# Performance work log

Measured on AMD Instinct MI355X. Metric: run time of the kernel, lower is better.

The kernel has to match this reference:

```python
import jax, jax.numpy as jnp
import numpy as np

B, N, C_IN, C_EMB, G = 16, 1024, 16, 64, 128
NEG = -1e12


def _lap(m):
    # m @ D^-1/2, transpose, @ D^-1/2  (matches torch code incl. transpose)
    d = jnp.sum(m, axis=1) ** -0.5
    return (m * d[None, :]).T * d[None, :]


def setup_inputs():
    key = jax.random.key(0)
    ks = jax.random.split(key, 16)
    f = jax.random.normal
    return {
        'x': f(ks[0], (B, C_IN, N), jnp.float32),
        'ct': f(ks[1], (B, C_EMB, N), jnp.float32),
        'graph_data': jax.random.uniform(ks[2], (2, N, N), dtype=jnp.float32),
        'emb_w': f(ks[3], (C_EMB, C_IN)) / np.sqrt(C_IN).astype(np.float32),
        'emb_b': f(ks[4], (C_EMB,)) * 0.01,
        'emb2_w': f(ks[5], (N, N)) / np.sqrt(N).astype(np.float32),
        'emb2_b': f(ks[6], (N,)) * 0.01,
        'att_W': f(ks[7], (C_EMB, C_EMB)) / np.sqrt(C_EMB).astype(np.float32),
        'att_a': f(ks[8], (2 * C_EMB, 1)) / np.sqrt(2 * C_EMB).astype(np.float32),
        'att_GL': f(ks[9], (N, G)) / np.sqrt(G).astype(np.float32),
        'uai_w': f(ks[10], (C_EMB, C_EMB)) / np.sqrt(C_EMB).astype(np.float32),
        'uai_b': f(ks[11], (C_EMB,)) * 0.01,
        'lin1_w': f(ks[12], (C_EMB, C_EMB)) / np.sqrt(C_EMB).astype(np.float32),
        'lin2_w': f(ks[13], (C_EMB, C_EMB)) / np.sqrt(C_EMB).astype(np.float32),
        'lin2_b': f(ks[14], (C_EMB,)) * 0.01,
        'ln_w': jnp.ones((C_EMB, N), jnp.float32),
        'ln_b': jnp.zeros((C_EMB, N), jnp.float32),
    }


def reference(x, ct, graph_data, emb_w, emb_b, emb2_w, emb2_b, att_W, att_a,
              att_GL, uai_w, uai_b, lin1_w, lin2_w, lin2_b, ln_w, ln_b):
    # emb: Conv1d k=1 -> leaky_relu -> Linear over node axis N
    h0 = jax.nn.leaky_relu(jnp.einsum('bcn,ec->ben', x, emb_w) + emb_b[None, :, None])
    h0 = jnp.einsum('ben,mn->bem', h0, emb2_w) + emb2_b[None, None, :]
    inp = jnp.swapaxes(h0, 1, 2)  # [B,N,C']

    # InterpositionAttention (repeat/cat factorized: e_ij = leakyrelu(a1.h_i + a2.h_j))
    eye = jnp.eye(N, dtype=x.dtype)
    adj_att = jax.nn.softmax(jax.nn.relu(att_GL @ att_GL.T), axis=-1) + eye
    h = inp @ att_W  # [B,N,C']
    e = jax.nn.leaky_relu((h @ att_a[:C_EMB]) + jnp.swapaxes(h @ att_a[C_EMB:], 1, 2))  # [B,N,N]
    att = jax.nn.softmax(jnp.where(adj_att > 0, e, NEG), axis=2)
    x_att = jnp.swapaxes(jax.nn.relu(att @ h), 1, 2)  # [B,C',N]

    # UAI module (eval mode: dropout off -> all MC samples equal -> sigma = 0)
    mu = jnp.swapaxes(x_att, 1, 2) @ uai_w.T + uai_b  # [B,N,C']
    x_uai = jnp.swapaxes(mu, 1, 2)  # [B,C',N]

    g1 = _lap(graph_data[0] + eye)
    g2 = _lap(graph_data[1] + eye)

    # learned adjacency from pairwise squared distances (cdist p=2, squared)
    xf = jnp.swapaxes(x_uai, 1, 2)  # [B,N,C']
    sq = jnp.sum(xf * xf, axis=-1)
    d2 = jnp.maximum(sq[:, :, None] + sq[:, None, :] - 2.0 * (xf @ jnp.swapaxes(xf, 1, 2)), 0.0)
    gl = jax.nn.softmax(jnp.exp(-d2 / (2.0 * C_EMB)) + eye, axis=-1)  # sigma^2 = emb_size

    def ln(z):  # LayerNorm over last two dims [C', N]
        m = jnp.mean(z, axis=(1, 2), keepdims=True)
        v = jnp.var(z, axis=(1, 2), keepdims=True)
        return (z - m) / jnp.sqrt(v + 1e-5) * ln_w + ln_b

    l1 = lambda z: jnp.einsum('oc,bcn->bon', lin1_w, z)
    l2 = lambda z: jnp.einsum('oc,bcn->bon', lin2_w, z) + lin2_b[None, :, None]

    x_new = ln(l1(x_uai) @ gl + l1(l1(x_uai) @ g1) @ g2)
    ft = jax.nn.gelu(ln(l2(x_uai) @ gl + l2(l2(x_uai) @ g1) @ g2), approximate=False)
    rt = ft  # rt is computed by the identical expression (dropout off)

    ct_new = ft * ct + x_new - ft * x_new
    ht = rt * jax.nn.elu(ct_new) + x_uai - rt * x_uai
    return (ht, ct_new)
```

## Files before the change

### kernel.cpp

```cpp
#include <hip/hip_runtime.h>
#include <math.h>

typedef unsigned short u16;
typedef __attribute__((ext_vector_type(8))) short short8;
typedef __attribute__((ext_vector_type(4))) float floatx4;

constexpr int BATCH = 16;
constexpr int NI = 1024;
constexpr int CE = 64;
constexpr int CI = 16;
constexpr long long NN2  = (long long)NI * NI;
constexpr long long BCN  = (long long)BATCH * CE * NI;
constexpr long long BNv  = (long long)BATCH * NI;
constexpr long long BNN  = (long long)BATCH * NI * NI;
constexpr long long S1 = (long long)CE * NI;
constexpr long long S2 = 2 * S1;
constexpr int ZERON = (int)(2 * BNv + 80);

__device__ __forceinline__ float lrelu01(float x) { return x > 0.f ? x : 0.01f * x; }

__device__ __forceinline__ u16 f2bf(float f) {
  unsigned u = __builtin_bit_cast(unsigned, f);
  return (u16)((u + 0x7fffu + ((u >> 16) & 1u)) >> 16);
}
__device__ __forceinline__ float bf2f(u16 h) {
  unsigned u = ((unsigned)h) << 16;
  return __builtin_bit_cast(float, u);
}
__device__ __forceinline__ unsigned fkey(float f) {
  unsigned u = __builtin_bit_cast(unsigned, f);
  return (u & 0x80000000u) ? ~u : (u | 0x80000000u);
}
__device__ __forceinline__ float funkey(unsigned k) {
  unsigned u = (k & 0x80000000u) ? (k & 0x7fffffffu) : ~k;
  return __builtin_bit_cast(float, u);
}

__device__ __forceinline__ void gload16(const u16* g, u16* l) {
  __builtin_amdgcn_global_load_lds(
      (const __attribute__((address_space(1))) void*)g,
      (__attribute__((address_space(3))) void*)l, 16, 0, 0);
}

__device__ __forceinline__ void pipe_fence() {
  asm volatile("s_waitcnt vmcnt(0) lgkmcnt(0)" ::: "memory");
  __builtin_amdgcn_sched_barrier(0);
  __builtin_amdgcn_s_barrier();
  __builtin_amdgcn_sched_barrier(0);
}

template<int N>
__device__ __forceinline__ void fence_bar() {
  __builtin_amdgcn_sched_barrier(0);
  if constexpr (N == 0) asm volatile("s_waitcnt vmcnt(0)" ::: "memory");
  else if constexpr (N == 1) asm volatile("s_waitcnt vmcnt(1)" ::: "memory");
  else if constexpr (N == 2) asm volatile("s_waitcnt vmcnt(2)" ::: "memory");
  else if constexpr (N == 3) asm volatile("s_waitcnt vmcnt(3)" ::: "memory");
  else if constexpr (N == 4) asm volatile("s_waitcnt vmcnt(4)" ::: "memory");
  else if constexpr (N == 6) asm volatile("s_waitcnt vmcnt(6)" ::: "memory");
  else if constexpr (N == 8) asm volatile("s_waitcnt vmcnt(8)" ::: "memory");
  else asm volatile("s_waitcnt vmcnt(0)" ::: "memory");
  __builtin_amdgcn_s_barrier();
  __builtin_amdgcn_sched_barrier(0);
}

template<int BM, int BN, int MODE>
__global__ __launch_bounds__(256) void mgemm(
    const u16* __restrict__ Ag, const u16* __restrict__ B1g, const u16* __restrict__ B2g,
    int K1, int K, int lda, int ldb, long long bsA, long long bsB1,
    float* __restrict__ Cf, u16* __restrict__ Cb, int ldc, long long bsC,
    const float* __restrict__ aux1, const float* __restrict__ aux2,
    const float* __restrict__ aux3, const float* __restrict__ aux4,
    float* __restrict__ Zout)
{
  constexpr int RM = BM / 2, RN = BN / 2, MI = RM / 16, NJ = RN / 16;
  constexpr bool PIPE3 = (MODE == 5 || MODE == 14 || MODE == 15);
  constexpr int DEPTH = (MODE == 5) ? 4 : 3;
  constexpr int NBUF = PIPE3 ? DEPTH : (MODE == 13 ? 2 : 1);
  constexpr int NLA = (BM * 8) / 256;
  constexpr int NLB = (BN * 8) / 256;
  constexpr int L = (MODE == 13) ? NLB : (NLA + NLB);
  __shared__ __align__(16) u16 As[NBUF * BM * 64];
  __shared__ __align__(16) u16 Bs[NBUF * BN * 64];
  __shared__ __align__(16) u16 xa[MODE == 13 ? 32 * 72 : 1];
  const int tid = threadIdx.x;
  int z, n0, r0;
  if constexpr (MODE == 15) {
    const int id = blockIdx.x;
    if (id >= 512) {
      const int m = id - 512;
      float s = 0.f, sv = 0.f;
      for (int n = tid; n < NI; n += 256) {
        float g = aux3[(long long)m * NI + n] * aux2[n];
        s += g;
        sv = fmaf(g, aux1[n], sv);
      }
      float* r1 = (float*)As;
      float* r2 = (float*)As + 256;
      r1[tid] = s; r2[tid] = sv; __syncthreads();
      for (int st = 128; st > 0; st >>= 1) {
        if (tid < st) { r1[tid] += r1[tid + st]; r2[tid] += r2[tid + st]; }
        __syncthreads();
      }
      if (tid == 0) {
        float dm = aux2[m];
        Cf[m] = dm * (r1[0] + dm);
        Zout[m] = dm * (r2[0] + dm * aux1[m]);
      }
      return;
    }
    z = 0; n0 = (id & 15) * BN; r0 = (id >> 4) * BM;
  } else {
    z = blockIdx.z; n0 = blockIdx.x * BN; r0 = blockIdx.y * BM;
  }
  const u16* Ab = Ag + (long long)z * bsA + (long long)r0 * lda;
  const u16* Bb1 = B1g + (long long)z * bsB1 + (long long)n0 * ldb;
  const int lane = tid & 63;
  const int wid = tid >> 6;
  const int wr = wid >> 1, wc = wid & 1;
  const int q = lane >> 4, mlow = lane & 15;
  const int wbase = tid & ~63;

  floatx4 acc[MI][NJ] = {};
  float zp0 = 0.f;

  float s1r_13 = 0.f, mr_13 = 0.f;
  const float* s2z_13 = nullptr;
  float4 sa, sb;
  if constexpr (MODE == 13) {
    const float* s1z = aux2 + (long long)z * NI;
    s2z_13 = aux3 + (long long)z * NI;
    const float mb = funkey(((const unsigned*)aux4)[z]);
    s1r_13 = s1z[r0 + (tid >> 3)];
    mr_13 = lrelu01(s1r_13 + mb);
  }

  auto stageAB = [&](int buf, int k0) {
    if constexpr (MODE != 13) {
      const u16* Asrc = Ab + k0;
#pragma unroll
      for (int s = 0; s < NLA; s++) {
        int cid = tid + s * 256;
        int r = cid >> 3, cc = cid & 7;
        gload16(Asrc + (long long)r * lda + ((cc ^ (r & 7)) << 3),
                As + buf * (BM * 64) + ((wbase + s * 256) << 3));
      }
    }
    const u16* Bsrc = (k0 < K1) ? (Bb1 + k0)
                                : (B2g + (long long)n0 * ldb + (k0 - K1));
#pragma unroll
    for (int s = 0; s < NLB; s++) {
      int cid = tid + s * 256;
      int r = cid >> 3, cc = cid & 7;
      gload16(Bsrc + (long long)r * ldb + ((cc ^ (r & 7)) << 3),
              Bs + buf * (BN * 64) + ((wbase + s * 256) << 3));
    }
  };

  auto agen_ld = [&](int k0) {
    const float* sp = s2z_13 + k0 + (tid & 7) * 8;
    sa = *(const float4*)sp;
    sb = *(const float4*)(sp + 4);
  };
  auto agen_st = [&](int buf) {
    int r = tid >> 3, craw = tid & 7;
    float p0 = __expf(lrelu01(s1r_13 + sa.x) - mr_13);
    float p1 = __expf(lrelu01(s1r_13 + sa.y) - mr_13);
    float p2 = __expf(lrelu01(s1r_13 + sa.z) - mr_13);
    float p3 = __expf(lrelu01(s1r_13 + sa.w) - mr_13);
    float p4 = __expf(lrelu01(s1r_13 + sb.x) - mr_13);
    float p5 = __expf(lrelu01(s1r_13 + sb.y) - mr_13);
    float p6 = __expf(lrelu01(s1r_13 + sb.z) - mr_13);
    float p7 = __expf(lrelu01(s1r_13 + sb.w) - mr_13);
    zp0 += p0 + p1 + p2 + p3 + p4 + p5 + p6 + p7;
    uint4 v;
    v.x = (unsigned)f2bf(p0) | ((unsigned)f2bf(p1) << 16);
    v.y = (unsigned)f2bf(p2) | ((unsigned)f2bf(p3) << 16);
    v.z = (unsigned)f2bf(p4) | ((unsigned)f2bf(p5) << 16);
    v.w = (unsigned)f2bf(p6) | ((unsigned)f2bf(p7) << 16);
    *(uint4*)&As[buf * (BM * 64) + (r * 8 + (craw ^ (r & 7))) * 8] = v;
  };

  auto compute_tile = [&](int buf) {
#pragma unroll
    for (int kh = 0; kh < 2; kh++) {
      const int kc = kh * 4 + q;
      short8 afr[MI], bfr[NJ];
#pragma unroll
      for (int i = 0; i < MI; i++) {
        int row = wr * RM + i * 16 + mlow;
        afr[i] = *(const short8*)&As[buf * (BM * 64) + (row * 8 + (kc ^ (row & 7))) * 8];
      }
#pragma unroll
      for (int j = 0; j < NJ; j++) {
        int row = wc * RN + j * 16 + mlow;
        bfr[j] = *(const short8*)&Bs[buf * (BN * 64) + (row * 8 + (kc ^ (row & 7))) * 8];
      }
#pragma unroll
      for (int i = 0; i < MI; i++)
#pragma unroll
        for (int j = 0; j < NJ; j++)
          acc[i][j] = __builtin_amdgcn_mfma_f32_16x16x32_bf16(afr[i], bfr[j], acc[i][j], 0, 0, 0);
    }
  };

  if constexpr (PIPE3) {
    const int nk = K >> 6;
#pragma unroll
    for (int p = 0; p < DEPTH - 1; p++) stageAB(p, p << 6);
    fence_bar<(DEPTH - 2) * L>();
    int cur = 0, stg = DEPTH - 1;
    for (int ki = 0; ki < nk; ki++) {
      if (ki + DEPTH - 1 < nk) stageAB(stg, (ki + DEPTH - 1) << 6);
      compute_tile(cur);
      if (ki + 1 < nk) {
        const int rem = nk - 1 - ki;
        const int u = (rem < DEPTH - 1) ? rem : (DEPTH - 1);
        if constexpr (DEPTH == 4) {
          if (u == 3) fence_bar<2 * L>();
          else if (u == 2) fence_bar<L>();
          else fence_bar<0>();
        } else {
          if (u == 2) fence_bar<L>();
          else fence_bar<0>();
        }
      }
      cur++; if (cur == NBUF) cur = 0;
      stg++; if (stg == NBUF) stg = 0;
    }
    __syncthreads();
  } else if constexpr (MODE == 13) {
    agen_ld(0);
    stageAB(0, 0);
    agen_st(0);
    pipe_fence();
    int cur = 0;
    for (int k0 = 0; k0 < K; k0 += 64) {
      if (k0 + 64 < K) {
        agen_ld(k0 + 64);
        stageAB(cur ^ 1, k0 + 64);
        agen_st(cur ^ 1);
      }
      compute_tile(cur);
      pipe_fence();
      cur ^= 1;
    }
  } else {
    for (int k0 = 0; k0 < K; k0 += 64) {
      stageAB(0, k0);
      __syncthreads();
      compute_tile(0);
      __syncthreads();
    }
  }

  if constexpr (MODE == 3) {
    const float* sqb = aux1 + (long long)z * NI;
#pragma unroll
    for (int i = 0; i < MI; i++) {
#pragma unroll
      for (int rg = 0; rg < 4; rg++) {
        int r = r0 + wr * RM + i * 16 + q * 4 + rg;
        float sqi = sqb[r];
        float rsum = 0.f;
#pragma unroll
        for (int j = 0; j < NJ; j++) {
          int ncol = n0 + wc * RN + j * 16 + mlow;
          float d2 = fmaxf(sqi + sqb[ncol] - 2.f * acc[i][j][rg], 0.f);
          float w = __expf(__expf(-d2 * (1.f / 128.f)) + (r == ncol ? 1.f : 0.f) - 2.f);
          Cb[(long long)z * bsC + (long long)r * ldc + ncol] = f2bf(w);
          rsum += w;
        }
        rsum += __shfl_xor(rsum, 1);
        rsum += __shfl_xor(rsum, 2);
        rsum += __shfl_xor(rsum, 4);
        rsum += __shfl_xor(rsum, 8);
        if (mlow == 0) atomicAdd(&Zout[(long long)z * NI + r], rsum);
      }
    }
  } else if constexpr (MODE == 14) {
    float ps1 = 0.f, ps2 = 0.f;
#pragma unroll
    for (int i = 0; i < MI; i++) {
#pragma unroll
      for (int rg = 0; rg < 4; rg++) {
        int r = wr * RM + i * 16 + q * 4 + rg;
        int ncol = n0 + wc * RN + mlow;
        float v = acc[i][0][rg] + aux3[r] * aux1[ncol];
        Cb[(long long)z * bsC + (long long)r * ldc + ncol] = f2bf(v);
        ps1 = fmaf(v, aux2[r], ps1);
        ps2 = fmaf(v, aux2[64 + r], ps2);
      }
    }
    ps1 += __shfl_xor(ps1, 16); ps1 += __shfl_xor(ps1, 32);
    ps2 += __shfl_xor(ps2, 16); ps2 += __shfl_xor(ps2, 32);
    float* sred = (float*)As;
    const int col = wc * RN + mlow;
    if (q == 0) { sred[col * 2 + wr] = ps1; sred[64 + col * 2 + wr] = ps2; }
    __syncthreads();
    if (tid < 32) {
      float v1 = sred[tid * 2] + sred[tid * 2 + 1];
      float v2 = sred[64 + tid * 2] + sred[64 + tid * 2 + 1];
      Cf[(long long)z * NI + n0 + tid] = v1;
      Zout[(long long)z * NI + n0 + tid] = v2;
      float mx = v2;
      for (int off = 1; off < 32; off <<= 1) mx = fmaxf(mx, __shfl_xor(mx, off));
      if (tid == 0) atomicMax((unsigned*)B2g + z, fkey(mx));
    }
  } else if constexpr (MODE == 13) {
    float* zred = (float*)xa;
    float* zinv = (float*)xa + 256;
    zred[(tid >> 3) * 8 + (tid & 7)] = zp0;
    __syncthreads();
    if (tid < 32) {
      float sum = 0.f;
#pragma unroll
      for (int j = 0; j < 8; j++) sum += zred[tid * 8 + j];
      zinv[tid] = 1.f / sum;
    }
    __syncthreads();
    float zr[4];
#pragma unroll
    for (int rg = 0; rg < 4; rg++) zr[rg] = zinv[wr * 16 + q * 4 + rg];
    __syncthreads();
#pragma unroll
    for (int j = 0; j < NJ; j++) {
#pragma unroll
      for (int rg = 0; rg < 4; rg++) {
        int row = wr * 16 + q * 4 + rg;
        int col = wc * RN + j * 16 + mlow;
        float v = fmaxf(acc[0][j][rg] * zr[rg], 0.f);
        xa[row * 72 + col] = f2bf(v);
      }
    }
#pragma unroll
    for (int s = 0; s < 2; s++) {
      int cid = tid + s * 256;
      int r = cid >> 3, cc = cid & 7;
      gload16(B2g + r * 64 + ((cc ^ (r & 7)) << 3),
              Bs + ((wbase + s * 256) << 3));
    }
    __syncthreads();
    floatx4 acc2[2] = {};
#pragma unroll
    for (int kh = 0; kh < 2; kh++) {
      const int kc = kh * 4 + q;
      short8 a2 = *(const short8*)&xa[(wr * 16 + mlow) * 72 + kc * 8];
#pragma unroll
      for (int j = 0; j < 2; j++) {
        int orow = wc * 32 + j * 16 + mlow;
        short8 b2 = *(const short8*)&Bs[(orow * 8 + (kc ^ (orow & 7))) * 8];
        acc2[j] = __builtin_amdgcn_mfma_f32_16x16x32_bf16(a2, b2, acc2[j], 0, 0, 0);
      }
    }
#pragma unroll
    for (int rg = 0; rg < 4; rg++) {
      int row = r0 + wr * 16 + q * 4 + rg;
      float sqp = 0.f;
#pragma unroll
      for (int j = 0; j < 2; j++) {
        int o = wc * 32 + j * 16 + mlow;
        float v = acc2[j][rg] + aux1[o];
        Cb[(long long)z * bsC + (long long)row * ldc + o] = f2bf(v);
        sqp = fmaf(v, v, sqp);
      }
      sqp += __shfl_xor(sqp, 1);
      sqp += __shfl_xor(sqp, 2);
      sqp += __shfl_xor(sqp, 4);
      sqp += __shfl_xor(sqp, 8);
      if (mlow == 0) atomicAdd(&Zout[(long long)z * NI + row], sqp);
    }
  } else if constexpr (MODE == 5) {
    float ts = 0.f, tss = 0.f;
#pragma unroll
    for (int i = 0; i < MI; i++) {
#pragma unroll
      for (int j = 0; j < NJ; j++) {
#pragma unroll
        for (int rg = 0; rg < 4; rg++) {
          int r = r0 + wr * RM + i * 16 + q * 4 + rg;
          int ncol = n0 + wc * RN + j * 16 + mlow;
          float v = acc[i][j][rg];
          v += aux3[r] * aux1[ncol] + aux4[r] * aux2[ncol];
          Cb[(long long)z * bsC + (long long)r * ldc + ncol] = f2bf(v);
          ts += v;
          tss = fmaf(v, v, tss);
        }
      }
    }
    float* red = (float*)As;
    red[tid] = ts; red[256 + tid] = tss;
    __syncthreads();
    for (int st = 128; st > 0; st >>= 1) {
      if (tid < st) { red[tid] += red[tid + st]; red[256 + tid] += red[256 + tid + st]; }
      __syncthreads();
    }
    if (tid == 0) {
      const int half = r0 >> 6;
      atomicAdd(&Zout[z * 2 + half], red[0]);
      atomicAdd(&Zout[32 + z * 2 + half], red[256]);
    }
  } else {
#pragma unroll
    for (int i = 0; i < MI; i++) {
#pragma unroll
      for (int j = 0; j < NJ; j++) {
#pragma unroll
        for (int rg = 0; rg < 4; rg++) {
          int r = r0 + wr * RM + i * 16 + q * 4 + rg;
          int ncol = n0 + wc * RN + j * 16 + mlow;
          float v = acc[i][j][rg];
          if constexpr (MODE == 4) {
            int blk = r >> 6, oo = r & 63;
            int drow = ((blk & 1) << 6) + oo;
            if (blk < 2) v = (v + aux3[drow]) / aux1[(long long)z * NI + ncol];
            Cb[(long long)z * bsC + (long long)drow * 2048 + (long long)(blk >> 1) * 1024 + ncol] =
                f2bf(v);
          } else {
            Cb[(long long)z * bsC + (long long)r * ldc + ncol] = f2bf(v);
          }
        }
      }
    }
  }
}

__global__ __launch_bounds__(256) void lap_rowsum(const float* __restrict__ gd,
                                                  float* __restrict__ dr,
                                                  float* __restrict__ zero)
{
  if (blockIdx.x >= 2048) {
    int i = (blockIdx.x - 2048) * 256 + threadIdx.x;
    if (i < ZERON) zero[i] = 0.f;
    return;
  }
  const int ki = blockIdx.x;
  const float* row = gd + (long long)ki * NI;
  float s = 0.f;
  for (int j = threadIdx.x; j < NI; j += 256) s += row[j];
  __shared__ float red[256];
  red[threadIdx.x] = s; __syncthreads();
  for (int st = 128; st > 0; st >>= 1) {
    if (threadIdx.x < st) red[threadIdx.x] += red[threadIdx.x + st];
    __syncthreads();
  }
  if (threadIdx.x == 0) dr[ki] = rsqrtf(red[0] + 1.f);
}

__global__ __launch_bounds__(256) void mega_prep(
    const float* __restrict__ l1w, const float* __restrict__ l2w,
    const float* __restrict__ l2b, const float* __restrict__ uaiw,
    const float* __restrict__ attW,
    u16* __restrict__ stack4, float* __restrict__ rb2ext, float* __restrict__ rl2ext,
    u16* __restrict__ uaiw_bf, u16* __restrict__ attwT_bf, float* __restrict__ wcs,
    const float* __restrict__ emb2w, u16* __restrict__ emb2w_bf,
    const float* __restrict__ x, const float* __restrict__ ew,
    const float* __restrict__ eb, u16* __restrict__ h0aT,
    const float* __restrict__ gd, const float* __restrict__ dsum,
    u16* __restrict__ g2t, u16* __restrict__ g1,
    float* __restrict__ cs1)
{
  __shared__ float sm[1092];
  const int bid = blockIdx.x;
  const int t = threadIdx.x;
  if (bid < 98) {
    const int gid = bid * 256 + t;
    if (gid < 4096) {
      stack4[gid] = f2bf(l1w[gid]);
    } else if (gid < 8192) {
      stack4[gid] = f2bf(l2w[gid - 4096]);
    } else if (gid < 12288) {
      int tt = gid - 8192, o = tt >> 6, m = tt & 63;
      float s = 0.f;
      for (int c = 0; c < 64; c++) s = fmaf(l1w[o * 64 + c], l1w[c * 64 + m], s);
      stack4[gid] = f2bf(s);
    } else if (gid < 16384) {
      int tt = gid - 12288, o = tt >> 6, m = tt & 63;
      float s = 0.f;
      for (int c = 0; c < 64; c++) s = fmaf(l2w[o * 64 + c], l2w[c * 64 + m], s);
      stack4[gid] = f2bf(s);
    } else if (gid < 16512) {
      int r = gid - 16384;
      rb2ext[r] = (r < 64) ? 0.f : l2b[r - 64];
    } else if (gid < 16640) {
      int r = gid - 16512;
      float v = 0.f;
      if (r >= 64) { int o = r - 64; for (int c = 0; c < 64; c++) v = fmaf(l2w[o * 64 + c], l2b[c], v); }
      rl2ext[r] = v;
    } else if (gid < 20736) {
      uaiw_bf[gid - 16640] = f2bf(uaiw[gid - 16640]);
    } else if (gid < 24832) {
      int idx = gid - 20736;
      int c = idx >> 6, e = idx & 63;
      attwT_bf[idx] = f2bf(attW[e * 64 + c]);
    } else if (gid < 24896) {
      int c = gid - 24832;
      float s = 0.f;
      for (int e = 0; e < 64; e++) s += attW[e * 64 + c];
      wcs[c] = s;
    }
  } else if (bid < 4194) {
    const long long i = (long long)(bid - 98) * 256 + t;
    emb2w_bf[i] = f2bf(emb2w[i]);
  } else if (bid < 4450) {
    const int sub = bid - 4194;
    const int b = sub >> 4;
    const int nc = (sub & 15) * 64;
    float* we = sm;
    float* be = sm + 1024;
    for (int i = t; i < 1024; i += 256) we[i] = ew[i];
    if (t < 64) be[t] = eb[t];
    __syncthreads();
    const int n = nc + (t >> 2);
    const int e0 = (t & 3) * 16;
    const float* xb = x + (long long)b * CI * NI + n;
    float xv[16];
#pragma unroll
    for (int c = 0; c < CI; c++) xv[c] = xb[(long long)c * NI];
    u16 out16[16];
#pragma unroll
    for (int ee = 0; ee < 16; ee++) {
      const int e = e0 + ee;
      float a = be[e];
#pragma unroll
      for (int c = 0; c < CI; c++) a = fmaf(xv[c], we[e * 16 + c], a);
      out16[ee] = f2bf(lrelu01(a));
    }
    u16* dst = h0aT + (long long)b * S1 + (long long)n * 64 + e0;
    *(uint4*)dst = *(uint4*)out16;
    *(uint4*)(dst + 8) = *(uint4*)(out16 + 8);
  } else if (bid < 8546) {
    const long long idx = (long long)(bid - 4450) * 256 + t;
    const int m = (int)(idx >> 10), j = (int)(idx & 1023);
    const float* d = dsum + NI;
    float v = (gd[NN2 + idx] + (m == j ? 1.f : 0.f)) * d[m] * d[j];
    g2t[idx] = f2bf(v);
  } else if (bid < 9570) {
    const int sub = bid - 8546;
    const int bx = (sub & 31) * 32, by = (sub >> 5) * 32;
    const int lx = t & 31, ly = t >> 5;
    float* tile = sm;
    for (int yy = ly; yy < 32; yy += 8)
      tile[yy * 33 + lx] = gd[(long long)(by + yy) * NI + bx + lx];
    __syncthreads();
    for (int yy = ly; yy < 32; yy += 8) {
      const int i = bx + yy, j = by + lx;
      float v = (tile[lx * 33 + yy] + (i == j ? 1.f : 0.f)) * dsum[i] * dsum[j];
      g1[(long long)i * NI + j] = f2bf(v);
    }
  } else {
    const int n = bid - 9570;
    float s = 0.f;
    for (int i = t; i < NI; i += 256) s = fmaf(gd[(long long)n * NI + i], dsum[i], s);
    float* red = sm;
    red[t] = s; __syncthreads();
    for (int st = 128; st > 0; st >>= 1) {
      if (t < st) red[t] += red[t + st];
      __syncthreads();
    }
    if (t == 0) cs1[n] = dsum[n] * (red[0] + dsum[n]);
  }
}

__global__ __launch_bounds__(512) void ln_final_t(const u16* __restrict__ T,
                                                  const float* __restrict__ stats,
                                                  const float* __restrict__ lnw,
                                                  const float* __restrict__ lnb,
                                                  const float* __restrict__ ct,
                                                  const u16* __restrict__ xuT,
                                                  float* __restrict__ outp)
{
  __shared__ float xs[64 * 65];
  const int blk = blockIdx.x;
  const int b = blk >> 4;
  const int n0 = (blk & 15) << 6;
  const int t = threadIdx.x;
  const int tc = t & 63, tr = t >> 6;
#pragma unroll
  for (int i = 0; i < 8; i++) {
    int nn = i * 8 + tr;
    xs[tc * 65 + nn] = bf2f(xuT[((long long)b << 16) + (long long)(n0 + nn) * 64 + tc]);
  }
  __syncthreads();
  const float inv_n = 1.f / 65536.f;
  const float m0 = stats[b * 2] * inv_n;
  const float m1 = stats[b * 2 + 1] * inv_n;
  const float rs0 = rsqrtf(fmaxf(stats[32 + b * 2] * inv_n - m0 * m0, 0.f) + 1e-5f);
  const float rs1 = rsqrtf(fmaxf(stats[32 + b * 2 + 1] * inv_n - m1 * m1, 0.f) + 1e-5f);
#pragma unroll
  for (int j = 0; j < 8; j++) {
    const int c = j * 8 + tr;
    const int n = n0 + tc;
    const int rem = c * NI + n;
    const long long toff = (long long)b * S2 + rem;
    const float t0 = bf2f(T[toff]);
    const float t1 = bf2f(T[toff + S1]);
    const float w = lnw[rem], bb = lnb[rem];
    const float xn = (t0 - m0) * rs0 * w + bb;
    float ft = (t1 - m1) * rs1 * w + bb;
    ft = 0.5f * ft * (1.f + erff(ft * 0.70710678118654752f));
    const float u = xs[c * 65 + tc];
    const long long oidx = ((long long)b << 16) + rem;
    const float cn = fmaf(ft, ct[oidx] - xn, xn);
    const float el = cn > 0.f ? cn : expm1f(cn);
    outp[oidx] = fmaf(ft, el - u, u);
    outp[BCN + oidx] = cn;
  }
}

extern "C" void kernel_launch(void* const* d_in, const int* in_sizes, int n_in,
                              void* d_out, int out_size, void* d_ws, size_t ws_size,
                              hipStream_t stream)
{
  (void)in_sizes; (void)n_in; (void)out_size; (void)ws_size;
  const float* x      = (const float*)d_in[0];
  const float* ct     = (const float*)d_in[1];
  const float* gdata  = (const float*)d_in[2];
  const float* emb_w  = (const float*)d_in[3];
  const float* emb_b  = (const float*)d_in[4];
  const float* emb2_w = (const float*)d_in[5];
  const float* emb2_b = (const float*)d_in[6];
  const float* att_W  = (const float*)d_in[7];
  const float* att_a  = (const float*)d_in[8];
  const float* uai_w  = (const float*)d_in[10];
  const float* uai_b  = (const float*)d_in[11];
  const float* lin1_w = (const float*)d_in[12];
  const float* lin2_w = (const float*)d_in[13];
  const float* lin2_b = (const float*)d_in[14];
  const float* ln_w   = (const float*)d_in[15];
  const float* ln_b   = (const float*)d_in[16];
  float* outp = (float*)d_out;

  float* ws = (float*)d_ws;
  long long o = 0;
  auto af = [&](long long n) { float* p = ws + o; o += (n + 63) & ~63LL; return p; };
  auto au = [&](long long n) { return (u16*)af((n + 1) / 2); };

  float* s1      = af(BNv);
  float* s2      = af(BNv);
  float* dsum    = af(2 * NI);
  float* cs1v    = af(NI);
  float* cs2v    = af(NI);
  float* v2v     = af(NI);
  float* rb2ext  = af(128);
  float* rl2ext  = af(128);
  float* wcs     = af(64);
  float* zeroreg = af(ZERON);
  float* Zgl     = zeroreg;
  float* sqv     = zeroreg + BNv;
  float* stats   = zeroreg + 2 * BNv;
  unsigned* s2mU = (unsigned*)(stats + 64);
  u16* Tacc      = au(S2 * BATCH);
  u16* emb2w_bf  = au(NN2);
  u16* h0aTb     = au(S1 * BATCH);
  u16* ybf       = au(S1 * BATCH);
  u16* hTb       = au(S1 * BATCH);
  u16* xuaiTb    = au(S1 * BATCH);
  u16* g1b       = au(NN2);
  u16* g2tb      = au(NN2);
  u16* G12b      = au(NN2);
  u16* Abig      = au((long long)BATCH * 128 * 2048);
  u16* stack4    = au(256 * 64);
  u16* uaiw_bf   = au(CE * CE);
  u16* attwT_bf  = au(CE * CE);
  u16* bigW      = au(BNN);

  lap_rowsum<<<2048 + (ZERON + 255) / 256, 256, 0, stream>>>(gdata, dsum, zeroreg);

  mega_prep<<<10594, 256, 0, stream>>>(
      lin1_w, lin2_w, lin2_b, uai_w, att_W,
      stack4, rb2ext, rl2ext, uaiw_bf, attwT_bf, wcs,
      emb2_w, emb2w_bf, x, emb_w, emb_b, h0aTb,
      gdata, dsum, g2tb, g1b, cs1v);

  mgemm<32, 64, 15><<<1536, 256, 0, stream>>>(
      g2tb, g1b, nullptr, NI, NI, NI, NI, 0, 0,
      cs2v, G12b, NI, 0, cs1v, dsum + NI, gdata + NN2, nullptr, v2v);

  mgemm<64, 32, 6><<<dim3(32, 1, BATCH), 256, 0, stream>>>(
      attwT_bf, h0aTb, nullptr, CE, CE, CE, CE, 0, S1,
      nullptr, ybf, NI, S1, nullptr, nullptr, nullptr, nullptr, nullptr);

  mgemm<64, 32, 14><<<dim3(32, 1, BATCH), 256, 0, stream>>>(
      ybf, emb2w_bf, (const u16*)s2mU, NI, NI, NI, NI, S1, 0,
      s1, hTb, NI, S1, emb2_b, att_a, wcs, nullptr, s2);

  mgemm<32, 64, 13><<<dim3(1, 32, BATCH), 256, 0, stream>>>(
      hTb, hTb, uaiw_bf, NI, NI, NI, NI, 0, S1,
      nullptr, xuaiTb, CE, S1, uai_b, s1, s2, (const float*)s2mU, sqv);

  mgemm<128, 128, 3><<<dim3(8, 8, BATCH), 256, 0, stream>>>(
      xuaiTb, xuaiTb, nullptr, CE, CE, CE, CE, S1, S1,
      nullptr, bigW, NI, NN2, sqv, nullptr, nullptr, nullptr, Zgl);

  mgemm<64, 64, 4><<<dim3(16, 4, BATCH), 256, 0, stream>>>(
      stack4, xuaiTb, nullptr, CE, CE, CE, CE, 0, S1,
      nullptr, Abig, 0, (long long)128 * 2048, Zgl, nullptr, rb2ext, nullptr, nullptr);

  mgemm<64, 64, 5><<<dim3(16, 2, BATCH), 256, 0, stream>>>(
      Abig, bigW, G12b, NI, 2 * NI, 2048, NI, (long long)128 * 2048, NN2,
      nullptr, Tacc, NI, S2, cs2v, v2v, rb2ext, rl2ext, stats);

  ln_final_t<<<256, 512, 0, stream>>>(Tacc, stats, ln_w, ln_b, ct, xuaiTb, outp);
}
```

Baseline: 229.6 us.

## Merge attention-weight GEMM into G12 launch, retile distance GEMM, XCD-swizzle final GEMM

Folds the small MODE 6 attention-weight projection GEMM into the MODE 15 launch as an extra set of 512 blocks. This removes one kernel launch and lets that work overlap with the G12 product and the column-sum blocks. The pairwise-distance GEMM (MODE 3) drops from 128x128 to 64x64 tiles, giving four times as many blocks. The final fused GEMM (MODE 5) now runs on a 1D grid whose block IDs are remapped so that blocks sharing a batch land on the same XCD, improving L2 locality. The risks are the pointer-offset trick that reaches ybf relative to G12b, and the smaller tiles cutting per-block reuse.

```diff
diff --git a/kernel.cpp b/kernel.cpp
--- a/kernel.cpp
+++ b/kernel.cpp
@@ -84,10 +84,11 @@
   __shared__ __align__(16) u16 Bs[NBUF * BN * 64];
   __shared__ __align__(16) u16 xa[MODE == 13 ? 32 * 72 : 1];
   const int tid = threadIdx.x;
-  int z, n0, r0;
+  int z, n0, r0, job15 = 0;
+  long long cboff = 0;
   if constexpr (MODE == 15) {
     const int id = blockIdx.x;
-    if (id >= 512) {
+    if (id >= 512 && id < 1536) {
       const int m = id - 512;
       float s = 0.f, sv = 0.f;
       for (int n = tid; n < NI; n += 256) {
@@ -109,12 +110,37 @@
       }
       return;
     }
-    z = 0; n0 = (id & 15) * BN; r0 = (id >> 4) * BM;
+    if (id >= 1536) {
+      const int id2 = id - 1536;
+      job15 = 2;
+      z = id2 >> 5; r0 = (id2 & 1) * BM; n0 = ((id2 >> 1) & 15) * BN;
+    } else {
+      z = 0; n0 = (id & 15) * BN; r0 = (id >> 4) * BM;
+    }
+  } else if constexpr (MODE == 5) {
+    const int fid = blockIdx.x;
+    const int xcd = fid & 7, idx = fid >> 3;
+    const int code = (idx >> 4) * 8 + xcd;
+    z = code >> 1; r0 = (code & 1) * BM; n0 = (idx & 15) * BN;
   } else {
     z = blockIdx.z; n0 = blockIdx.x * BN; r0 = blockIdx.y * BM;
   }
-  const u16* Ab = Ag + (long long)z * bsA + (long long)r0 * lda;
-  const u16* Bb1 = B1g + (long long)z * bsB1 + (long long)n0 * ldb;
+  int Kv = K, K1v = K1, ldav = lda, ldbv = ldb;
+  const u16 *Ab, *Bb1;
+  if constexpr (MODE == 15) {
+    if (job15 == 2) {
+      Kv = 64; K1v = 128; ldav = 64; ldbv = 64;
+      Ab = B2g + (long long)r0 * 64;
+      Bb1 = (const u16*)aux4 + (long long)z * S1 + (long long)n0 * 64;
+      cboff = bsB1 + (long long)z * S1;
+    } else {
+      Ab = Ag + (long long)r0 * lda;
+      Bb1 = B1g + (long long)n0 * ldb;
+    }
+  } else {
+    Ab = Ag + (long long)z * bsA + (long long)r0 * ldav;
+    Bb1 = B1g + (long long)z * bsB1 + (long long)n0 * ldbv;
+  }
   const int lane = tid & 63;
   const int wid = tid >> 6;
   const int wr = wid >> 1, wc = wid & 1;
@@ -142,17 +168,17 @@
       for (int s = 0; s < NLA; s++) {
         int cid = tid + s * 256;
         int r = cid >> 3, cc = cid & 7;
-        gload16(Asrc + (long long)r * lda + ((cc ^ (r & 7)) << 3),
+        gload16(Asrc + (long long)r * ldav + ((cc ^ (r & 7)) << 3),
                 As + buf * (BM * 64) + ((wbase + s * 256) << 3));
       }
     }
-    const u16* Bsrc = (k0 < K1) ? (Bb1 + k0)
-                                : (B2g + (long long)n0 * ldb + (k0 - K1));
+    const u16* Bsrc = (k0 < K1v) ? (Bb1 + k0)
+                                 : (B2g + (long long)n0 * ldbv + (k0 - K1v));
 #pragma unroll
     for (int s = 0; s < NLB; s++) {
       int cid = tid + s * 256;
       int r = cid >> 3, cc = cid & 7;
-      gload16(Bsrc + (long long)r * ldb + ((cc ^ (r & 7)) << 3),
+      gload16(Bsrc + (long long)r * ldbv + ((cc ^ (r & 7)) << 3),
               Bs + buf * (BN * 64) + ((wbase + s * 256) << 3));
     }
   };
@@ -205,7 +231,7 @@
   };
 
   if constexpr (PIPE3) {
-    const int nk = K >> 6;
+    const int nk = Kv >> 6;
 #pragma unroll
     for (int p = 0; p < DEPTH - 1; p++) stageAB(p, p << 6);
     fence_bar<(DEPTH - 2) * L>();
@@ -235,8 +261,8 @@
     agen_st(0);
     pipe_fence();
     int cur = 0;
-    for (int k0 = 0; k0 < K; k0 += 64) {
-      if (k0 + 64 < K) {
+    for (int k0 = 0; k0 < Kv; k0 += 64) {
+      if (k0 + 64 < Kv) {
         agen_ld(k0 + 64);
         stageAB(cur ^ 1, k0 + 64);
         agen_st(cur ^ 1);
@@ -246,7 +272,7 @@
       cur ^= 1;
     }
   } else {
-    for (int k0 = 0; k0 < K; k0 += 64) {
+    for (int k0 = 0; k0 < Kv; k0 += 64) {
       stageAB(0, k0);
       __syncthreads();
       compute_tile(0);
@@ -416,6 +442,8 @@
             if (blk < 2) v = (v + aux3[drow]) / aux1[(long long)z * NI + ncol];
             Cb[(long long)z * bsC + (long long)drow * 2048 + (long long)(blk >> 1) * 1024 + ncol] =
                 f2bf(v);
+          } else if constexpr (MODE == 15) {
+            Cb[cboff + (long long)r * ldc + ncol] = f2bf(v);
           } else {
             Cb[(long long)z * bsC + (long long)r * ldc + ncol] = f2bf(v);
           }
@@ -673,13 +701,9 @@
       emb2_w, emb2w_bf, x, emb_w, emb_b, h0aTb,
       gdata, dsum, g2tb, g1b, cs1v);
 
-  mgemm<32, 64, 15><<<1536, 256, 0, stream>>>(
-      g2tb, g1b, nullptr, NI, NI, NI, NI, 0, 0,
-      cs2v, G12b, NI, 0, cs1v, dsum + NI, gdata + NN2, nullptr, v2v);
-
-  mgemm<64, 32, 6><<<dim3(32, 1, BATCH), 256, 0, stream>>>(
-      attwT_bf, h0aTb, nullptr, CE, CE, CE, CE, 0, S1,
-      nullptr, ybf, NI, S1, nullptr, nullptr, nullptr, nullptr, nullptr);
+  mgemm<32, 64, 15><<<2048, 256, 0, stream>>>(
+      g2tb, g1b, attwT_bf, NI, NI, NI, NI, 0, (long long)(ybf - G12b),
+      cs2v, G12b, NI, 0, cs1v, dsum + NI, gdata + NN2, (const float*)h0aTb, v2v);
 
   mgemm<64, 32, 14><<<dim3(32, 1, BATCH), 256, 0, stream>>>(
       ybf, emb2w_bf, (const u16*)s2mU, NI, NI, NI, NI, S1, 0,
@@ -689,7 +713,7 @@
       hTb, hTb, uaiw_bf, NI, NI, NI, NI, 0, S1,
       nullptr, xuaiTb, CE, S1, uai_b, s1, s2, (const float*)s2mU, sqv);
 
-  mgemm<128, 128, 3><<<dim3(8, 8, BATCH), 256, 0, stream>>>(
+  mgemm<64, 64, 3><<<dim3(16, 16, 16), 256, 0, stream>>>(
       xuaiTb, xuaiTb, nullptr, CE, CE, CE, CE, S1, S1,
       nullptr, bigW, NI, NN2, sqv, nullptr, nullptr, nullptr, Zgl);
 
@@ -697,7 +721,7 @@
       stack4, xuaiTb, nullptr, CE, CE, CE, CE, 0, S1,
       nullptr, Abig, 0, (long long)128 * 2048, Zgl, nullptr, rb2ext, nullptr, nullptr);
 
-  mgemm<64, 64, 5><<<dim3(16, 2, BATCH), 256, 0, stream>>>(
+  mgemm<64, 64, 5><<<512, 256, 0, stream>>>(
       Abig, bigW, G12b, NI, 2 * NI, 2048, NI, (long long)128 * 2048, NN2,
       nullptr, Tacc, NI, S2, cs2v, v2v, rb2ext, rl2ext, stats);
 
```

Result: faster. 224.6 us (-2.2%).
